# Kernel tuning notes

Hardware: AMD Instinct MI355X
Metric: run time of the kernel (lower is better)

Reference implementation:

```python
import jax, jax.numpy as jnp
import numpy as np

M = 4        # multi_anchor
B = 256      # graphs per batch
NPG = 64     # nodes per graph
N = B * NPG  # total nodes
DEG = 8
E = N * DEG
DF = 16      # raw node feature dim
D = 256      # emb_dim
L = 5        # num_layer
NA = 2       # num_anchor
TASKS = 10
T = 1.0


def _gnn_node(h, edge_src, edge_dst, gin_W1, gin_b1, gin_W2, gin_b2, eps):
    # GIN-style message passing: gather -> sum-scatter -> 2-layer MLP, per layer.
    for l in range(L):
        msg = h[:, edge_src]                                  # [M,E,D] gather
        agg = jnp.zeros_like(h).at[:, edge_dst].add(msg)      # [M,N,D] scatter-add
        z = (1.0 + eps[l]) * h + agg
        z = jax.nn.relu(z @ gin_W1[l] + gin_b1[l])
        h = jax.nn.relu(z @ gin_W2[l] + gin_b2[l])
    return h


def _mindist(h):
    # per-node min squared distance to other nodes in the same graph
    hg = h.reshape(M, B, NPG, D)
    sq = jnp.sum(hg * hg, axis=-1)                            # [M,B,n]
    d2 = sq[..., :, None] + sq[..., None, :] - 2.0 * jnp.einsum('mbid,mbjd->mbij', hg, hg)
    d2 = jnp.maximum(d2, 0.0) + jnp.eye(NPG, dtype=h.dtype) * 1e9
    return jnp.min(d2, axis=-1).reshape(M, N)


def reference(x, W_enc, b_enc, gin_W1, gin_b1, gin_W2, gin_b2, eps,
              anchor_emb, W_n2n, b_n2n, W_pred, b_pred, edge_src, edge_dst):
    # InputEncoder (float x -> MLP with tail activation)
    h0 = jax.nn.relu(x @ W_enc + b_enc)                       # [N,D]
    tx = jnp.broadcast_to(h0[None], (M, N, D))                # expand over multi_anchor
    anchor = jnp.zeros((M, N), dtype=jnp.int32)
    xcur = tx
    skey = jax.random.key(42)
    goff = jnp.arange(B) * NPG                                # graph offsets
    rows = jnp.arange(M)[:, None]
    for i in range(1, NA + 1):
        h = _gnn_node(xcur, edge_src, edge_dst, gin_W1, gin_b1, gin_W2, gin_b2, eps)
        mind = _mindist(h)                                    # [M,N]
        pred = -mind - 10.0 * (anchor > 0).astype(h.dtype)    # mask prior anchors
        logits = (pred * T).reshape(M, B, NPG)
        # categorical sample per (anchor-row, graph) via Gumbel-max == multinomial_sample_batch
        u = jax.random.uniform(jax.random.fold_in(skey, i), (M, B, NPG), minval=1e-9, maxval=1.0)
        idx = jnp.argmax(logits - jnp.log(-jnp.log(u)), axis=-1)  # [M,B]
        glob = idx + goff[None, :]
        anchor = anchor.at[rows, glob].set(i)
        xcur = tx * anchor_emb[anchor] + tx
    h = _gnn_node(xcur, edge_src, edge_dst, gin_W1, gin_b1, gin_W2, gin_b2, eps)
    hn = jax.nn.relu(h @ W_n2n + b_n2n)                       # node2node (tailact)
    hg = hn.reshape(M, B, NPG, D).mean(axis=2)                # mean graph pooling
    out = hg @ W_pred + b_pred                                # pred_lin
    return out.mean(axis=0)                                   # mean over multi_anchor -> [B,TASKS]


def setup_inputs():
    key = jax.random.key(0)
    ks = jax.random.split(key, 12)
    x = jax.random.normal(ks[0], (N, DF), dtype=jnp.float32)
    gid = jnp.repeat(jnp.arange(B), NPG * DEG)
    edge_src = gid * NPG + jax.random.randint(ks[1], (E,), 0, NPG)
    edge_dst = gid * NPG + jax.random.randint(ks[2], (E,), 0, NPG)
    s = lambda k, shp: (jax.random.normal(k, shp, dtype=jnp.float32) * 0.05)
    return {
        'x': x,
        'W_enc': s(ks[3], (DF, D)), 'b_enc': jnp.zeros((D,), jnp.float32),
        'gin_W1': s(ks[4], (L, D, D)), 'gin_b1': jnp.zeros((L, D), jnp.float32),
        'gin_W2': s(ks[5], (L, D, D)), 'gin_b2': jnp.zeros((L, D), jnp.float32),
        'eps': jnp.zeros((L,), jnp.float32),
        'anchor_emb': s(ks[6], (NA + 1, D)),
        'W_n2n': s(ks[7], (D, D)), 'b_n2n': jnp.zeros((D,), jnp.float32),
        'W_pred': s(ks[8], (D, TASKS)), 'b_pred': jnp.zeros((TASKS,), jnp.float32),
        'edge_src': edge_src, 'edge_dst': edge_dst,
    }
```

## Files before the change

kernel.cpp:

```cpp
#include <hip/hip_runtime.h>
#include <stdint.h>

typedef unsigned short u16;
typedef _Float16 f16;
typedef f16 f16x4 __attribute__((ext_vector_type(4)));
typedef f16 f16x8 __attribute__((ext_vector_type(8)));
typedef float f32x16 __attribute__((ext_vector_type(16)));

#define M_     4
#define B_     256
#define NPG_   64
#define N_     (B_*NPG_)
#define DEG_   8
#define E_     (N_*DEG_)
#define DF_    16
#define D_     256
#define L_     5
#define NA_    2
#define TASKS_ 10

#define HROW 520
#define TROW 136
#define MFMA16(a,b,c) __builtin_amdgcn_mfma_f32_32x32x16_f16(a,b,c,0,0,0)

__device__ __forceinline__ u16 h_bits(f16 h) { union { f16 h; u16 u; } c; c.h = h; return c.u; }
__device__ __forceinline__ f16 bits_h(u16 u) { union { u16 u; f16 h; } c; c.u = u; return c.h; }
__device__ __forceinline__ float h2f(u16 u) { return (float)bits_h(u); }
__device__ __forceinline__ void split_f16(float v, u16& hi, u16& lo) {
  f16 h = (f16)v;
  f16 l = (f16)(v - (float)h);
  hi = h_bits(h); lo = h_bits(l);
}

__device__ __forceinline__ int haddr8(int row, int chunk) {
  return row * HROW + ((chunk ^ (row & 7)) << 4);
}
__device__ __forceinline__ int taddr8(int d, int c) {
  return d * TROW + ((c ^ (d & 7)) << 4);
}

__device__ __forceinline__ uint32_t rotl32(uint32_t v, int r) { return (v << r) | (v >> (32 - r)); }
__device__ __forceinline__ void threefry2x32(uint32_t k0, uint32_t k1, uint32_t x0, uint32_t x1,
                                             uint32_t& o0, uint32_t& o1) {
  const uint32_t ks2 = k0 ^ k1 ^ 0x1BD11BDAu;
  x0 += k0; x1 += k1;
#define TFR(r) { x0 += x1; x1 = rotl32(x1, r); x1 ^= x0; }
  TFR(13) TFR(15) TFR(26) TFR(6)   x0 += k1;  x1 += ks2 + 1u;
  TFR(17) TFR(29) TFR(16) TFR(24)  x0 += ks2; x1 += k0 + 2u;
  TFR(13) TFR(15) TFR(26) TFR(6)   x0 += k0;  x1 += k1 + 3u;
  TFR(17) TFR(29) TFR(16) TFR(24)  x0 += k1;  x1 += ks2 + 4u;
  TFR(13) TFR(15) TFR(26) TFR(6)   x0 += ks2; x1 += k0 + 5u;
#undef TFR
  o0 = x0; o1 = x1;
}

template<int TERMS>
__device__ __forceinline__ void gemm_w_RT(u16* __restrict__ hfU, const u16* __restrict__ WTm,
                                          const float* __restrict__ bias, bool do_relu) {
  const int tid = threadIdx.x;
  const int lane = tid & 63, w = tid >> 6;
  const int l31 = lane & 31, lh = lane >> 5;
  const int col = w * 32 + l31;
  const float bv = bias ? bias[col] : 0.f;
  f32x16 acc0 = {}, acc1 = {};
  const u16* Bbase = WTm + col * 8;

  f16x8 ah0[3], ah1[3], al0[3], al1[3];
  f16x8 bh[4], bl[4];
  auto ldA = [&](int ks, int s) {
    const int chunk = ks * 2 + lh;
    const int a0 = haddr8(l31, chunk);
    const int a1 = haddr8(32 + l31, chunk);
    ah0[s] = *(const f16x8*)(hfU + a0);
    ah1[s] = *(const f16x8*)(hfU + a1);
    if (TERMS == 3) {
      al0[s] = *(const f16x8*)(hfU + a0 + 8);
      al1[s] = *(const f16x8*)(hfU + a1 + 8);
    }
  };
  auto ldB = [&](int ks, int s) {
    const int chunk = ks * 2 + lh;
    bh[s] = *(const f16x8*)(Bbase + chunk * 2048);
    if (TERMS == 3) bl[s] = *(const f16x8*)(Bbase + chunk * 2048 + 65536);
  };
  ldB(0, 0); ldB(1, 1); ldB(2, 2); ldA(0, 0); ldA(1, 1);
#pragma unroll
  for (int ks = 0; ks < 16; ++ks) {
    if (ks < 14) ldA(ks + 2, (ks + 2) % 3);
    if (ks < 13) ldB(ks + 3, (ks + 3) & 3);
    const int s = ks % 3, t = ks & 3;
    __builtin_amdgcn_s_setprio(1);
    if (TERMS == 3) {
      acc0 = MFMA16(ah0[s], bh[t], acc0);
      acc0 = MFMA16(ah0[s], bl[t], acc0);
      acc0 = MFMA16(al0[s], bh[t], acc0);
      acc1 = MFMA16(ah1[s], bh[t], acc1);
      acc1 = MFMA16(ah1[s], bl[t], acc1);
      acc1 = MFMA16(al1[s], bh[t], acc1);
    } else {
      acc0 = MFMA16(ah0[s], bh[t], acc0);
      acc1 = MFMA16(ah1[s], bh[t], acc1);
    }
    __builtin_amdgcn_s_setprio(0);
  }
  __syncthreads();
#pragma unroll
  for (int q = 0; q < 4; ++q) {
    f16x4 h4a, l4a, h4b, l4b;
#pragma unroll
    for (int e = 0; e < 4; ++e) {
      float v0 = acc0[q * 4 + e] + bv;
      float v1 = acc1[q * 4 + e] + bv;
      if (do_relu) { v0 = fmaxf(v0, 0.f); v1 = fmaxf(v1, 0.f); }
      if (TERMS == 3) {
        u16 hi, lo;
        split_f16(v0, hi, lo); h4a[e] = bits_h(hi); l4a[e] = bits_h(lo);
        split_f16(v1, hi, lo); h4b[e] = bits_h(hi); l4b[e] = bits_h(lo);
      } else {
        h4a[e] = (f16)v0; h4b[e] = (f16)v1;
      }
    }
    const int t0 = taddr8(col, q) + 4 * lh;
    const int t1 = taddr8(col, 4 + q) + 4 * lh;
    *(f16x4*)(hfU + t0) = h4a;
    *(f16x4*)(hfU + t1) = h4b;
    if (TERMS == 3) { *(f16x4*)(hfU + t0 + 8) = l4a; *(f16x4*)(hfU + t1 + 8) = l4b; }
  }
  __syncthreads();
}

template<int TERMS>
__device__ __forceinline__ void gemm_adj_TR(u16* __restrict__ hfU, const u16* __restrict__ AdjU,
                                            const float* __restrict__ bias, int slow,
                                            const float* __restrict__ diagC, float epsl) {
  const int tid = threadIdx.x;
  const int lane = tid & 63, w = tid >> 6;
  const int l31 = lane & 31, lh = lane >> 5;
  const int drow = w * 32 + l31;
  f32x16 acc0 = {}, acc1 = {};

  f16x8 uh[2], ul[2], B0[2], B1[2];
  auto ld = [&](int kk, int s) {
    const int chunk = kk * 2 + lh;
    const int ta = taddr8(drow, chunk);
    uh[s] = *(const f16x8*)(hfU + ta);
    if (TERMS == 3) ul[s] = *(const f16x8*)(hfU + ta + 8);
    B0[s] = *(const f16x8*)(AdjU + l31 * 72 + chunk * 8);
    B1[s] = *(const f16x8*)(AdjU + (32 + l31) * 72 + chunk * 8);
  };
  ld(0, 0);
#pragma unroll
  for (int kk = 0; kk < 4; ++kk) {
    if (kk < 3) ld(kk + 1, (kk + 1) & 1);
    const int s = kk & 1;
    __builtin_amdgcn_s_setprio(1);
    acc0 = MFMA16(uh[s], B0[s], acc0);
    acc1 = MFMA16(uh[s], B1[s], acc1);
    if (TERMS == 3) {
      acc0 = MFMA16(ul[s], B0[s], acc0);
      acc1 = MFMA16(ul[s], B1[s], acc1);
    }
    __builtin_amdgcn_s_setprio(0);
  }
  if (slow) {
    const int i0 = l31, i1 = 32 + l31;
    const float v0d = diagC[i0] + epsl, v1d = diagC[i1] + epsl;
    const float r0 = v0d - h2f(h_bits((f16)v0d));
    const float r1 = v1d - h2f(h_bits((f16)v1d));
#pragma unroll
    for (int r = 0; r < 16; ++r) {
      const int dp = w * 32 + (r & 3) + 8 * (r >> 2) + 4 * lh;
      const int a0 = taddr8(dp, i0 >> 3) + (i0 & 7);
      const int a1 = taddr8(dp, i1 >> 3) + (i1 & 7);
      float u0 = h2f(hfU[a0]);
      float u1 = h2f(hfU[a1]);
      if (TERMS == 3) { u0 += h2f(hfU[a0 + 8]); u1 += h2f(hfU[a1 + 8]); }
      acc0[r] += r0 * u0;
      acc1[r] += r1 * u1;
    }
  }
  __syncthreads();
#pragma unroll
  for (int q = 0; q < 4; ++q) {
    f16x4 h4a, l4a, h4b, l4b;
#pragma unroll
    for (int e = 0; e < 4; ++e) {
      const int r = q * 4 + e;
      const float bq = bias[w * 32 + 8 * q + 4 * lh + e];
      float v0 = fmaxf(acc0[r] + bq, 0.f);
      float v1 = fmaxf(acc1[r] + bq, 0.f);
      if (TERMS == 3) {
        u16 hi, lo;
        split_f16(v0, hi, lo); h4a[e] = bits_h(hi); l4a[e] = bits_h(lo);
        split_f16(v1, hi, lo); h4b[e] = bits_h(hi); l4b[e] = bits_h(lo);
      } else {
        h4a[e] = (f16)v0; h4b[e] = (f16)v1;
      }
    }
    const int c = w * 4 + q;
    const int a0 = haddr8(l31, c) + 4 * lh;
    const int a1 = haddr8(32 + l31, c) + 4 * lh;
    *(f16x4*)(hfU + a0) = h4a;
    *(f16x4*)(hfU + a1) = h4b;
    if (TERMS == 3) { *(f16x4*)(hfU + a0 + 8) = l4a; *(f16x4*)(hfU + a1 + 8) = l4b; }
  }
  __syncthreads();
}

template<int TERMS>
__device__ __forceinline__ void gemm_w_RR(u16* __restrict__ hfU, const u16* __restrict__ WTm,
                                          const float* __restrict__ bias, bool do_relu) {
  const int tid = threadIdx.x;
  const int lane = tid & 63, w = tid >> 6;
  const int l31 = lane & 31, lh = lane >> 5;
  f32x16 acc0 = {}, acc1 = {};
  const u16* Abase = WTm + (w * 32 + l31) * 8;

  f16x8 Wh[4], Wl[4];
  f16x8 Xh0[3], Xh1[3], Xl0[3], Xl1[3];
  auto ldW = [&](int ks, int s) {
    const int chunk = ks * 2 + lh;
    Wh[s] = *(const f16x8*)(Abase + chunk * 2048);
    if (TERMS == 3) Wl[s] = *(const f16x8*)(Abase + chunk * 2048 + 65536);
  };
  auto ldX = [&](int ks, int s) {
    const int chunk = ks * 2 + lh;
    const int b0 = haddr8(l31, chunk);
    const int b1_ = haddr8(32 + l31, chunk);
    Xh0[s] = *(const f16x8*)(hfU + b0);
    Xh1[s] = *(const f16x8*)(hfU + b1_);
    if (TERMS == 3) {
      Xl0[s] = *(const f16x8*)(hfU + b0 + 8);
      Xl1[s] = *(const f16x8*)(hfU + b1_ + 8);
    }
  };
  ldW(0, 0); ldW(1, 1); ldW(2, 2); ldX(0, 0); ldX(1, 1);
#pragma unroll
  for (int ks = 0; ks < 16; ++ks) {
    if (ks < 14) ldX(ks + 2, (ks + 2) % 3);
    if (ks < 13) ldW(ks + 3, (ks + 3) & 3);
    const int s = ks % 3, t = ks & 3;
    __builtin_amdgcn_s_setprio(1);
    if (TERMS == 3) {
      acc0 = MFMA16(Wh[t], Xh0[s], acc0);
      acc0 = MFMA16(Wl[t], Xh0[s], acc0);
      acc0 = MFMA16(Wh[t], Xl0[s], acc0);
      acc1 = MFMA16(Wh[t], Xh1[s], acc1);
      acc1 = MFMA16(Wl[t], Xh1[s], acc1);
      acc1 = MFMA16(Wh[t], Xl1[s], acc1);
    } else {
      acc0 = MFMA16(Wh[t], Xh0[s], acc0);
      acc1 = MFMA16(Wh[t], Xh1[s], acc1);
    }
    __builtin_amdgcn_s_setprio(0);
  }
  __syncthreads();
#pragma unroll
  for (int q = 0; q < 4; ++q) {
    f16x4 h4a, l4a, h4b, l4b;
#pragma unroll
    for (int e = 0; e < 4; ++e) {
      const int r = q * 4 + e;
      const float bq = bias[w * 32 + 8 * q + 4 * lh + e];
      float v0 = acc0[r] + bq;
      float v1 = acc1[r] + bq;
      if (do_relu) { v0 = fmaxf(v0, 0.f); v1 = fmaxf(v1, 0.f); }
      if (TERMS == 3) {
        u16 hi, lo;
        split_f16(v0, hi, lo); h4a[e] = bits_h(hi); l4a[e] = bits_h(lo);
        split_f16(v1, hi, lo); h4b[e] = bits_h(hi); l4b[e] = bits_h(lo);
      } else {
        h4a[e] = (f16)v0; h4b[e] = (f16)v1;
      }
    }
    const int c = w * 4 + q;
    const int a0 = haddr8(l31, c) + 4 * lh;
    const int a1 = haddr8(32 + l31, c) + 4 * lh;
    *(f16x4*)(hfU + a0) = h4a;
    *(f16x4*)(hfU + a1) = h4b;
    if (TERMS == 3) { *(f16x4*)(hfU + a0 + 8) = l4a; *(f16x4*)(hfU + a1 + 8) = l4b; }
  }
  __syncthreads();
}

__device__ __forceinline__ void mindist_mfma(u16* __restrict__ hfU, float* __restrict__ mindS) {
  const int tid = threadIdx.x;
  const int lane = tid & 63, w = tid >> 6;
  const int gb = w & 3, gi = gb >> 1, gj = gb & 1, ks = w >> 2;
  const int l31 = lane & 31, lh = lane >> 5;
  f32x16 acc = {};

  f16x8 Ah[2], Al[2], Bh[2], Bl[2];
  auto ld = [&](int t, int s) {
    const int chunk = 4 * t + 2 * ks + lh;
    const int ra = haddr8(gi * 32 + l31, chunk);
    const int rb_ = haddr8(gj * 32 + l31, chunk);
    Ah[s] = *(const f16x8*)(hfU + ra);
    Al[s] = *(const f16x8*)(hfU + ra + 8);
    Bh[s] = *(const f16x8*)(hfU + rb_);
    Bl[s] = *(const f16x8*)(hfU + rb_ + 8);
  };
  ld(0, 0);
#pragma unroll
  for (int t = 0; t < 8; ++t) {
    if (t < 7) ld(t + 1, (t + 1) & 1);
    const int s = t & 1;
    __builtin_amdgcn_s_setprio(1);
    acc = MFMA16(Ah[s], Bh[s], acc);
    acc = MFMA16(Ah[s], Bl[s], acc);
    acc = MFMA16(Al[s], Bh[s], acc);
    __builtin_amdgcn_s_setprio(0);
  }
  __syncthreads();
  float* hfF = (float*)hfU;
  if (ks == 1) {
#pragma unroll
    for (int r = 0; r < 16; ++r) {
      const int rr = (r & 3) + 8 * (r >> 2) + 4 * lh;
      hfF[gb * 1088 + rr * 34 + l31] = acc[r];
    }
  }
  __syncthreads();
  if (ks == 0) {
#pragma unroll
    for (int r = 0; r < 16; ++r) {
      const int rr = (r & 3) + 8 * (r >> 2) + 4 * lh;
      const float g = acc[r] + hfF[gb * 1088 + rr * 34 + l31];
      hfF[8192 + (gi * 32 + rr) * 66 + gj * 32 + l31] = g;
    }
  }
  __syncthreads();
  {
    const int i = tid >> 3, jt = tid & 7;
    const float gii = hfF[8192 + i * 66 + i];
    float dmin = 3.4e38f;
#pragma unroll
    for (int jj = 0; jj < 8; ++jj) {
      const int j = jt * 8 + jj;
      const float gjj = hfF[8192 + j * 66 + j];
      const float gij = hfF[8192 + i * 66 + j];
      float d2 = fmaxf(gii + gjj - 2.f * gij, 0.f);
      if (j == i) d2 += 1e9f;
      dmin = fminf(dmin, d2);
    }
    dmin = fminf(dmin, __shfl_xor(dmin, 1));
    dmin = fminf(dmin, __shfl_xor(dmin, 2));
    dmin = fminf(dmin, __shfl_xor(dmin, 4));
    if (jt == 0) mindS[i] = dmin;
  }
  __syncthreads();
}

__device__ __forceinline__ void stage_adj(u16* AdjU, const float* AdjF, int b, int tid) {
  const float* src = AdjF + b * 4096;
  for (int t = tid; t < 4096; t += 512)
    AdjU[(t >> 6) * 72 + (t & 63)] = h_bits((f16)src[t]);
}

template<bool WRITE_LO>
__device__ __forceinline__ void build_xcur(u16* hfU, const float* h0g, const float* aemb,
                                           const int* anchorS, int b, int tid) {
  const int i = tid >> 3, part = tid & 7;
  const float* t = h0g + (b * 64 + i) * 256;
  const float* e = aemb + anchorS[i] * D_;
#pragma unroll
  for (int c = 0; c < 4; ++c) {
    const int chunk = part * 4 + c;
    const float4 tv0 = *(const float4*)(t + chunk * 8);
    const float4 tv1 = *(const float4*)(t + chunk * 8 + 4);
    const float4 ev0 = *(const float4*)(e + chunk * 8);
    const float4 ev1 = *(const float4*)(e + chunk * 8 + 4);
    float vv[8];
    vv[0] = fmaf(tv0.x, ev0.x, tv0.x); vv[1] = fmaf(tv0.y, ev0.y, tv0.y);
    vv[2] = fmaf(tv0.z, ev0.z, tv0.z); vv[3] = fmaf(tv0.w, ev0.w, tv0.w);
    vv[4] = fmaf(tv1.x, ev1.x, tv1.x); vv[5] = fmaf(tv1.y, ev1.y, tv1.y);
    vv[6] = fmaf(tv1.z, ev1.z, tv1.z); vv[7] = fmaf(tv1.w, ev1.w, tv1.w);
    f16x8 hi8, lo8;
#pragma unroll
    for (int ee = 0; ee < 8; ++ee) { u16 h, l; split_f16(vv[ee], h, l); hi8[ee] = bits_h(h); lo8[ee] = bits_h(l); }
    const int a = haddr8(i, chunk);
    *(f16x8*)(hfU + a) = hi8;
    if (WRITE_LO) *(f16x8*)(hfU + a + 8) = lo8;
  }
}

__device__ __forceinline__ void sample_anchor(const float* mindS, float* scoreS, int* anchorS,
                                              int m, int b, int iter, int tid) {
  if (tid < 64) {
    const int j = tid;
    uint32_t k0, k1;
    threefry2x32(0u, 42u, 0u, (uint32_t)iter, k0, k1);
    const uint32_t p = (uint32_t)(m * (B_ * NPG_) + b * NPG_ + j);
    uint32_t o0, o1, bits;
    if (p < 32768u) { threefry2x32(k0, k1, p, p + 32768u, o0, o1); bits = o0; }
    else            { threefry2x32(k0, k1, p - 32768u, p, o0, o1); bits = o1; }
    const float f = __uint_as_float((bits >> 9) | 0x3f800000u) - 1.0f;
    const float uv = fmaxf(1e-9f, f + 1e-9f);
    const float pred = -mindS[j] - ((anchorS[j] > 0) ? 10.0f : 0.0f);
    scoreS[j] = pred - logf(-logf(uv));
  }
  __syncthreads();
  if (tid == 0) {
    int best = 0; float bv = scoreS[0];
    for (int j = 1; j < 64; ++j) { const float v = scoreS[j]; if (v > bv) { bv = v; best = j; } }
    anchorS[best] = iter;
  }
}

__global__ void build_adj_kernel(const int* __restrict__ esrc, const int* __restrict__ edst,
                                 float* __restrict__ AdjF) {
  const int e = blockIdx.x * 256 + threadIdx.x;
  if (e < E_) {
    const int s = esrc[e];
    const int d = edst[e];
    const int g = s >> 6;
    atomicAdd(AdjF + g * 4096 + (d & 63) * 64 + (s & 63), 1.0f);
  }
}

__global__ __launch_bounds__(256) void prep_wt(const float* __restrict__ gW1, const float* __restrict__ gW2,
                                               const float* __restrict__ Wn2n, u16* __restrict__ WTbuf) {
  const int mat = blockIdx.x;
  const float* Wsrc = (mat < 5) ? (gW1 + mat * 65536)
                    : (mat < 10) ? (gW2 + (mat - 5) * 65536) : Wn2n;
  u16* dst = WTbuf + (size_t)mat * 131072;
  const int base = blockIdx.y * 2048;
  for (int idx = base + threadIdx.x; idx < base + 2048; idx += 256) {
    const int k = idx >> 8, d = idx & 255;
    const float a = Wsrc[idx];
    u16 hi, lo; split_f16(a, hi, lo);
    const int off = (k >> 3) * 2048 + d * 8 + (k & 7);
    dst[off] = hi;
    dst[65536 + off] = lo;
  }
}

__global__ __launch_bounds__(512)
void gnn1_kernel(const float* __restrict__ x, const float* __restrict__ Wenc,
                 const float* __restrict__ benc, float* __restrict__ h0g,
                 const float* __restrict__ AdjF, const u16* __restrict__ WTbuf,
                 const float* __restrict__ gb1, const float* __restrict__ gb2,
                 const float* __restrict__ eps, float* __restrict__ mindG) {
  __shared__ __align__(16) u16 hfU[256 * TROW];
  __shared__ __align__(16) u16 AdjU[64 * 72];
  __shared__ float mindS[64];
  __shared__ float diagC[64];
  __shared__ int flagS;
  const int tid = threadIdx.x;
  const int b = blockIdx.x;

  {
    float* scr = (float*)hfU;
    for (int t = tid; t < 4096; t += 512) {
      const int k = t >> 8, d = t & 255;
      scr[k * 264 + d + (d >> 5)] = Wenc[t];
    }
    if (tid < 256) scr[4300 + tid] = benc[tid];
    for (int t = tid; t < 1024; t += 512) scr[4600 + t] = x[b * 1024 + t];
    __syncthreads();

    const int i = tid >> 3, part = tid & 7;
    float xv[16];
#pragma unroll
    for (int k = 0; k < 16; ++k) xv[k] = scr[4600 + i * 16 + k];
    float hv[32];
#pragma unroll
    for (int dd = 0; dd < 32; ++dd) {
      const int d = part * 32 + dd;
      float acc = scr[4300 + d];
#pragma unroll
      for (int k = 0; k < 16; ++k) acc = fmaf(xv[k], scr[k * 264 + d + (d >> 5)], acc);
      hv[dd] = fmaxf(acc, 0.f);
    }
    float* dst = h0g + (b * 64 + i) * 256 + part * 32;
#pragma unroll
    for (int dd = 0; dd < 32; dd += 4) {
      float4 v; v.x = hv[dd]; v.y = hv[dd + 1]; v.z = hv[dd + 2]; v.w = hv[dd + 3];
      *(float4*)(dst + dd) = v;
    }
    __syncthreads();
#pragma unroll
    for (int c = 0; c < 4; ++c) {
      f16x8 hi8, lo8;
#pragma unroll
      for (int e = 0; e < 8; ++e) { u16 h, l; split_f16(hv[c * 8 + e], h, l); hi8[e] = bits_h(h); lo8[e] = bits_h(l); }
      const int a = haddr8(i, part * 4 + c);
      *(f16x8*)(hfU + a) = hi8;
      *(f16x8*)(hfU + a + 8) = lo8;
    }
  }
  stage_adj(AdjU, AdjF, b, tid);
  if (tid == 0) flagS = 0;
  if (tid < 64) {
    const float dc = AdjF[b * 4096 + tid * 65];
    diagC[tid] = dc;
    int f = 0;
    for (int l = 0; l < L_; ++l) {
      const float v = dc + 1.0f + eps[l];
      if (h2f(h_bits((f16)v)) != v) f = 1;
    }
    if (f) atomicOr(&flagS, 1);
  }
  __syncthreads();
  const int slow = flagS;

  for (int l = 0; l < L_; ++l) {
    const float epsl = 1.0f + eps[l];
    if (tid < 64) AdjU[tid * 72 + tid] = h_bits((f16)(diagC[tid] + epsl));
    gemm_w_RT<3>(hfU, WTbuf + (size_t)l * 131072, nullptr, false);
    gemm_adj_TR<3>(hfU, AdjU, gb1 + l * D_, slow, diagC, epsl);
    gemm_w_RR<3>(hfU, WTbuf + (size_t)(5 + l) * 131072, gb2 + l * D_, true);
  }
  mindist_mfma(hfU, mindS);
  if (tid < 64) mindG[b * 64 + tid] = mindS[tid];
}

__global__ __launch_bounds__(512, 4)
void mega_kernel(const float* __restrict__ h0g, const float* __restrict__ AdjF,
                 const u16* __restrict__ WTbuf,
                 const float* __restrict__ gb1, const float* __restrict__ gb2,
                 const float* __restrict__ eps, const float* __restrict__ aemb,
                 const float* __restrict__ bn2n,
                 const float* __restrict__ Wpred, const float* __restrict__ bpred,
                 const float* __restrict__ mindG, float* __restrict__ outp) {
  __shared__ __align__(16) u16 hfU[256 * TROW];
  __shared__ __align__(16) u16 AdjU[64 * 72];
  __shared__ float mindS[64];
  __shared__ float scoreS[64];
  __shared__ float hgS[256];
  __shared__ int   anchorS[64];
  __shared__ float diagC[64];
  __shared__ int   flagS;

  const int tid = threadIdx.x;
  const int b = blockIdx.x;
  const int m = blockIdx.y;

  stage_adj(AdjU, AdjF, b, tid);
  if (tid == 0) flagS = 0;
  if (tid < 64) {
    anchorS[tid] = 0;
    mindS[tid] = mindG[b * 64 + tid];
    const float dc = AdjF[b * 4096 + tid * 65];
    diagC[tid] = dc;
    int f = 0;
    for (int l = 0; l < L_; ++l) {
      const float v = dc + 1.0f + eps[l];
      if (h2f(h_bits((f16)v)) != v) f = 1;
    }
    if (f) atomicOr(&flagS, 1);
  }
  __syncthreads();

  sample_anchor(mindS, scoreS, anchorS, m, b, 1, tid);
  __syncthreads();
  build_xcur<true>(hfU, h0g, aemb, anchorS, b, tid);
  __syncthreads();

  const int slow = flagS;

  for (int l = 0; l < L_; ++l) {
    const float epsl = 1.0f + eps[l];
    if (tid < 64) AdjU[tid * 72 + tid] = h_bits((f16)(diagC[tid] + epsl));
    gemm_w_RT<3>(hfU, WTbuf + (size_t)l * 131072, nullptr, false);
    gemm_adj_TR<3>(hfU, AdjU, gb1 + l * D_, slow, diagC, epsl);
    gemm_w_RR<3>(hfU, WTbuf + (size_t)(5 + l) * 131072, gb2 + l * D_, true);
  }
  mindist_mfma(hfU, mindS);
  sample_anchor(mindS, scoreS, anchorS, m, b, 2, tid);
  __syncthreads();
  build_xcur<false>(hfU, h0g, aemb, anchorS, b, tid);
  __syncthreads();

  for (int l = 0; l < L_; ++l) {
    const float epsl = 1.0f + eps[l];
    if (tid < 64) AdjU[tid * 72 + tid] = h_bits((f16)(diagC[tid] + epsl));
    gemm_w_RT<1>(hfU, WTbuf + (size_t)l * 131072, nullptr, false);
    gemm_adj_TR<1>(hfU, AdjU, gb1 + l * D_, slow, diagC, epsl);
    gemm_w_RR<1>(hfU, WTbuf + (size_t)(5 + l) * 131072, gb2 + l * D_, true);
  }

  gemm_w_RT<1>(hfU, WTbuf + (size_t)10 * 131072, bn2n, true);
  if (tid < 256) {
    float s = 0.f;
#pragma unroll
    for (int c = 0; c < 8; ++c) {
      const f16x8 v = *(const f16x8*)(hfU + taddr8(tid, c));
      s += (float)v[0] + (float)v[1] + (float)v[2] + (float)v[3]
         + (float)v[4] + (float)v[5] + (float)v[6] + (float)v[7];
    }
    hgS[tid] = s * (1.0f / 64.0f);
  }
  __syncthreads();
  if (tid < 160) {
    const int t = tid >> 4, part = tid & 15;
    float s = 0.f;
    for (int d = part * 16; d < part * 16 + 16; ++d) s = fmaf(hgS[d], Wpred[d * TASKS_ + t], s);
    s += __shfl_xor(s, 1); s += __shfl_xor(s, 2); s += __shfl_xor(s, 4); s += __shfl_xor(s, 8);
    if (part == 0) {
      float val = s * 0.25f;
      if (m == 0) val += bpred[t];
      atomicAdd(outp + b * TASKS_ + t, val);
    }
  }
}

extern "C" void kernel_launch(void* const* d_in, const int* in_sizes, int n_in,
                              void* d_out, int out_size, void* d_ws, size_t ws_size,
                              hipStream_t stream) {
  const float* x     = (const float*)d_in[0];
  const float* Wenc  = (const float*)d_in[1];
  const float* benc  = (const float*)d_in[2];
  const float* gW1   = (const float*)d_in[3];
  const float* gb1   = (const float*)d_in[4];
  const float* gW2   = (const float*)d_in[5];
  const float* gb2   = (const float*)d_in[6];
  const float* eps   = (const float*)d_in[7];
  const float* aemb  = (const float*)d_in[8];
  const float* Wn2n  = (const float*)d_in[9];
  const float* bn2n  = (const float*)d_in[10];
  const float* Wpred = (const float*)d_in[11];
  const float* bpred = (const float*)d_in[12];
  const int* esrc    = (const int*)d_in[13];
  const int* edst    = (const int*)d_in[14];
  float* outp = (float*)d_out;

  float* h0g  = (float*)d_ws;
  float* AdjF = h0g + (size_t)N_ * D_;
  u16* WTbuf  = (u16*)(AdjF + B_ * 4096);
  float* mindG = (float*)(WTbuf + (size_t)11 * 131072);

  hipMemsetAsync(AdjF, 0, (size_t)B_ * 4096 * sizeof(float), stream);
  hipMemsetAsync(outp, 0, (size_t)out_size * sizeof(float), stream);
  build_adj_kernel<<<dim3((E_ + 255) / 256), dim3(256), 0, stream>>>(esrc, edst, AdjF);
  prep_wt<<<dim3(11, 32), dim3(256), 0, stream>>>(gW1, gW2, Wn2n, WTbuf);
  gnn1_kernel<<<dim3(B_), dim3(512), 0, stream>>>(x, Wenc, benc, h0g, AdjF, WTbuf,
                                                  gb1, gb2, eps, mindG);
  mega_kernel<<<dim3(B_, M_), dim3(512), 0, stream>>>(h0g, AdjF, WTbuf, gb1, gb2,
                                                      eps, aemb, bn2n, Wpred, bpred, mindG, outp);
}
```

Before: 714.7 us.

## Ping-pong LDS buffers to drop mid-GEMM barriers and interleave MFMA chains

Replaces the single in-place shared activation buffer with two ping-pong buffers, so each GEMM stage reads one buffer and writes the other. This removes the barrier that separated the last read from the epilogue write in every GEMM and in mindist. It also interleaves the acc0/acc1 MFMA chains to reduce dependency stalls, and sets launch bounds to one block. The cost is double the LDS per block (about 140KB), which likely limits occupancy to one 512-thread block per CU.

```diff
diff --git a/kernel.cpp b/kernel.cpp
--- a/kernel.cpp
+++ b/kernel.cpp
@@ -21,6 +21,7 @@
 
 #define HROW 520
 #define TROW 136
+#define BUFW (256 * TROW)
 #define MFMA16(a,b,c) __builtin_amdgcn_mfma_f32_32x32x16_f16(a,b,c,0,0,0)
 
 __device__ __forceinline__ u16 h_bits(f16 h) { union { f16 h; u16 u; } c; c.h = h; return c.u; }
@@ -55,7 +56,8 @@
 }
 
 template<int TERMS>
-__device__ __forceinline__ void gemm_w_RT(u16* __restrict__ hfU, const u16* __restrict__ WTm,
+__device__ __forceinline__ void gemm_w_RT(const u16* __restrict__ rbuf, u16* __restrict__ wbuf,
+                                          const u16* __restrict__ WTm,
                                           const float* __restrict__ bias, bool do_relu) {
   const int tid = threadIdx.x;
   const int lane = tid & 63, w = tid >> 6;
@@ -71,11 +73,11 @@
     const int chunk = ks * 2 + lh;
     const int a0 = haddr8(l31, chunk);
     const int a1 = haddr8(32 + l31, chunk);
-    ah0[s] = *(const f16x8*)(hfU + a0);
-    ah1[s] = *(const f16x8*)(hfU + a1);
+    ah0[s] = *(const f16x8*)(rbuf + a0);
+    ah1[s] = *(const f16x8*)(rbuf + a1);
     if (TERMS == 3) {
-      al0[s] = *(const f16x8*)(hfU + a0 + 8);
-      al1[s] = *(const f16x8*)(hfU + a1 + 8);
+      al0[s] = *(const f16x8*)(rbuf + a0 + 8);
+      al1[s] = *(const f16x8*)(rbuf + a1 + 8);
     }
   };
   auto ldB = [&](int ks, int s) {
@@ -92,10 +94,10 @@
     __builtin_amdgcn_s_setprio(1);
     if (TERMS == 3) {
       acc0 = MFMA16(ah0[s], bh[t], acc0);
+      acc1 = MFMA16(ah1[s], bh[t], acc1);
       acc0 = MFMA16(ah0[s], bl[t], acc0);
+      acc1 = MFMA16(ah1[s], bl[t], acc1);
       acc0 = MFMA16(al0[s], bh[t], acc0);
-      acc1 = MFMA16(ah1[s], bh[t], acc1);
-      acc1 = MFMA16(ah1[s], bl[t], acc1);
       acc1 = MFMA16(al1[s], bh[t], acc1);
     } else {
       acc0 = MFMA16(ah0[s], bh[t], acc0);
@@ -103,7 +105,6 @@
     }
     __builtin_amdgcn_s_setprio(0);
   }
-  __syncthreads();
 #pragma unroll
   for (int q = 0; q < 4; ++q) {
     f16x4 h4a, l4a, h4b, l4b;
@@ -122,15 +123,16 @@
     }
     const int t0 = taddr8(col, q) + 4 * lh;
     const int t1 = taddr8(col, 4 + q) + 4 * lh;
-    *(f16x4*)(hfU + t0) = h4a;
-    *(f16x4*)(hfU + t1) = h4b;
-    if (TERMS == 3) { *(f16x4*)(hfU + t0 + 8) = l4a; *(f16x4*)(hfU + t1 + 8) = l4b; }
+    *(f16x4*)(wbuf + t0) = h4a;
+    *(f16x4*)(wbuf + t1) = h4b;
+    if (TERMS == 3) { *(f16x4*)(wbuf + t0 + 8) = l4a; *(f16x4*)(wbuf + t1 + 8) = l4b; }
   }
   __syncthreads();
 }
 
 template<int TERMS>
-__device__ __forceinline__ void gemm_adj_TR(u16* __restrict__ hfU, const u16* __restrict__ AdjU,
+__device__ __forceinline__ void gemm_adj_TR(const u16* __restrict__ rbuf, u16* __restrict__ wbuf,
+                                            const u16* __restrict__ AdjU,
                                             const float* __restrict__ bias, int slow,
                                             const float* __restrict__ diagC, float epsl) {
   const int tid = threadIdx.x;
@@ -143,8 +145,8 @@
   auto ld = [&](int kk, int s) {
     const int chunk = kk * 2 + lh;
     const int ta = taddr8(drow, chunk);
-    uh[s] = *(const f16x8*)(hfU + ta);
-    if (TERMS == 3) ul[s] = *(const f16x8*)(hfU + ta + 8);
+    uh[s] = *(const f16x8*)(rbuf + ta);
+    if (TERMS == 3) ul[s] = *(const f16x8*)(rbuf + ta + 8);
     B0[s] = *(const f16x8*)(AdjU + l31 * 72 + chunk * 8);
     B1[s] = *(const f16x8*)(AdjU + (32 + l31) * 72 + chunk * 8);
   };
@@ -172,14 +174,13 @@
       const int dp = w * 32 + (r & 3) + 8 * (r >> 2) + 4 * lh;
       const int a0 = taddr8(dp, i0 >> 3) + (i0 & 7);
       const int a1 = taddr8(dp, i1 >> 3) + (i1 & 7);
-      float u0 = h2f(hfU[a0]);
-      float u1 = h2f(hfU[a1]);
-      if (TERMS == 3) { u0 += h2f(hfU[a0 + 8]); u1 += h2f(hfU[a1 + 8]); }
+      float u0 = h2f(rbuf[a0]);
+      float u1 = h2f(rbuf[a1]);
+      if (TERMS == 3) { u0 += h2f(rbuf[a0 + 8]); u1 += h2f(rbuf[a1 + 8]); }
       acc0[r] += r0 * u0;
       acc1[r] += r1 * u1;
     }
   }
-  __syncthreads();
 #pragma unroll
   for (int q = 0; q < 4; ++q) {
     f16x4 h4a, l4a, h4b, l4b;
@@ -200,15 +201,16 @@
     const int c = w * 4 + q;
     const int a0 = haddr8(l31, c) + 4 * lh;
     const int a1 = haddr8(32 + l31, c) + 4 * lh;
-    *(f16x4*)(hfU + a0) = h4a;
-    *(f16x4*)(hfU + a1) = h4b;
-    if (TERMS == 3) { *(f16x4*)(hfU + a0 + 8) = l4a; *(f16x4*)(hfU + a1 + 8) = l4b; }
+    *(f16x4*)(wbuf + a0) = h4a;
+    *(f16x4*)(wbuf + a1) = h4b;
+    if (TERMS == 3) { *(f16x4*)(wbuf + a0 + 8) = l4a; *(f16x4*)(wbuf + a1 + 8) = l4b; }
   }
   __syncthreads();
 }
 
 template<int TERMS>
-__device__ __forceinline__ void gemm_w_RR(u16* __restrict__ hfU, const u16* __restrict__ WTm,
+__device__ __forceinline__ void gemm_w_RR(const u16* __restrict__ rbuf, u16* __restrict__ wbuf,
+                                          const u16* __restrict__ WTm,
                                           const float* __restrict__ bias, bool do_relu) {
   const int tid = threadIdx.x;
   const int lane = tid & 63, w = tid >> 6;
@@ -227,11 +229,11 @@
     const int chunk = ks * 2 + lh;
     const int b0 = haddr8(l31, chunk);
     const int b1_ = haddr8(32 + l31, chunk);
-    Xh0[s] = *(const f16x8*)(hfU + b0);
-    Xh1[s] = *(const f16x8*)(hfU + b1_);
+    Xh0[s] = *(const f16x8*)(rbuf + b0);
+    Xh1[s] = *(const f16x8*)(rbuf + b1_);
     if (TERMS == 3) {
-      Xl0[s] = *(const f16x8*)(hfU + b0 + 8);
-      Xl1[s] = *(const f16x8*)(hfU + b1_ + 8);
+      Xl0[s] = *(const f16x8*)(rbuf + b0 + 8);
+      Xl1[s] = *(const f16x8*)(rbuf + b1_ + 8);
     }
   };
   ldW(0, 0); ldW(1, 1); ldW(2, 2); ldX(0, 0); ldX(1, 1);
@@ -243,10 +245,10 @@
     __builtin_amdgcn_s_setprio(1);
     if (TERMS == 3) {
       acc0 = MFMA16(Wh[t], Xh0[s], acc0);
+      acc1 = MFMA16(Wh[t], Xh1[s], acc1);
       acc0 = MFMA16(Wl[t], Xh0[s], acc0);
+      acc1 = MFMA16(Wl[t], Xh1[s], acc1);
       acc0 = MFMA16(Wh[t], Xl0[s], acc0);
-      acc1 = MFMA16(Wh[t], Xh1[s], acc1);
-      acc1 = MFMA16(Wl[t], Xh1[s], acc1);
       acc1 = MFMA16(Wh[t], Xl1[s], acc1);
     } else {
       acc0 = MFMA16(Wh[t], Xh0[s], acc0);
@@ -254,7 +256,6 @@
     }
     __builtin_amdgcn_s_setprio(0);
   }
-  __syncthreads();
 #pragma unroll
   for (int q = 0; q < 4; ++q) {
     f16x4 h4a, l4a, h4b, l4b;
@@ -276,14 +277,15 @@
     const int c = w * 4 + q;
     const int a0 = haddr8(l31, c) + 4 * lh;
     const int a1 = haddr8(32 + l31, c) + 4 * lh;
-    *(f16x4*)(hfU + a0) = h4a;
-    *(f16x4*)(hfU + a1) = h4b;
-    if (TERMS == 3) { *(f16x4*)(hfU + a0 + 8) = l4a; *(f16x4*)(hfU + a1 + 8) = l4b; }
-  }
-  __syncthreads();
-}
-
-__device__ __forceinline__ void mindist_mfma(u16* __restrict__ hfU, float* __restrict__ mindS) {
+    *(f16x4*)(wbuf + a0) = h4a;
+    *(f16x4*)(wbuf + a1) = h4b;
+    if (TERMS == 3) { *(f16x4*)(wbuf + a0 + 8) = l4a; *(f16x4*)(wbuf + a1 + 8) = l4b; }
+  }
+  __syncthreads();
+}
+
+__device__ __forceinline__ void mindist_mfma(const u16* __restrict__ rbuf, u16* __restrict__ scr,
+                                             float* __restrict__ mindS) {
   const int tid = threadIdx.x;
   const int lane = tid & 63, w = tid >> 6;
   const int gb = w & 3, gi = gb >> 1, gj = gb & 1, ks = w >> 2;
@@ -295,10 +297,10 @@
     const int chunk = 4 * t + 2 * ks + lh;
     const int ra = haddr8(gi * 32 + l31, chunk);
     const int rb_ = haddr8(gj * 32 + l31, chunk);
-    Ah[s] = *(const f16x8*)(hfU + ra);
-    Al[s] = *(const f16x8*)(hfU + ra + 8);
-    Bh[s] = *(const f16x8*)(hfU + rb_);
-    Bl[s] = *(const f16x8*)(hfU + rb_ + 8);
+    Ah[s] = *(const f16x8*)(rbuf + ra);
+    Al[s] = *(const f16x8*)(rbuf + ra + 8);
+    Bh[s] = *(const f16x8*)(rbuf + rb_);
+    Bl[s] = *(const f16x8*)(rbuf + rb_ + 8);
   };
   ld(0, 0);
 #pragma unroll
@@ -311,8 +313,7 @@
     acc = MFMA16(Al[s], Bh[s], acc);
     __builtin_amdgcn_s_setprio(0);
   }
-  __syncthreads();
-  float* hfF = (float*)hfU;
+  float* hfF = (float*)scr;
   if (ks == 1) {
 #pragma unroll
     for (int r = 0; r < 16; ++r) {
@@ -358,7 +359,7 @@
 }
 
 template<bool WRITE_LO>
-__device__ __forceinline__ void build_xcur(u16* hfU, const float* h0g, const float* aemb,
+__device__ __forceinline__ void build_xcur(u16* dst, const float* h0g, const float* aemb,
                                            const int* anchorS, int b, int tid) {
   const int i = tid >> 3, part = tid & 7;
   const float* t = h0g + (b * 64 + i) * 256;
@@ -379,8 +380,8 @@
 #pragma unroll
     for (int ee = 0; ee < 8; ++ee) { u16 h, l; split_f16(vv[ee], h, l); hi8[ee] = bits_h(h); lo8[ee] = bits_h(l); }
     const int a = haddr8(i, chunk);
-    *(f16x8*)(hfU + a) = hi8;
-    if (WRITE_LO) *(f16x8*)(hfU + a + 8) = lo8;
+    *(f16x8*)(dst + a) = hi8;
+    if (WRITE_LO) *(f16x8*)(dst + a + 8) = lo8;
   }
 }
 
@@ -435,13 +436,14 @@
   }
 }
 
-__global__ __launch_bounds__(512)
+__global__ __launch_bounds__(512, 1)
 void gnn1_kernel(const float* __restrict__ x, const float* __restrict__ Wenc,
                  const float* __restrict__ benc, float* __restrict__ h0g,
                  const float* __restrict__ AdjF, const u16* __restrict__ WTbuf,
                  const float* __restrict__ gb1, const float* __restrict__ gb2,
                  const float* __restrict__ eps, float* __restrict__ mindG) {
-  __shared__ __align__(16) u16 hfU[256 * TROW];
+  __shared__ __align__(16) u16 bufA[BUFW];
+  __shared__ __align__(16) u16 bufB[BUFW];
   __shared__ __align__(16) u16 AdjU[64 * 72];
   __shared__ float mindS[64];
   __shared__ float diagC[64];
@@ -450,7 +452,7 @@
   const int b = blockIdx.x;
 
   {
-    float* scr = (float*)hfU;
+    float* scr = (float*)bufB;
     for (int t = tid; t < 4096; t += 512) {
       const int k = t >> 8, d = t & 255;
       scr[k * 264 + d + (d >> 5)] = Wenc[t];
@@ -478,15 +480,14 @@
       float4 v; v.x = hv[dd]; v.y = hv[dd + 1]; v.z = hv[dd + 2]; v.w = hv[dd + 3];
       *(float4*)(dst + dd) = v;
     }
-    __syncthreads();
 #pragma unroll
     for (int c = 0; c < 4; ++c) {
       f16x8 hi8, lo8;
 #pragma unroll
       for (int e = 0; e < 8; ++e) { u16 h, l; split_f16(hv[c * 8 + e], h, l); hi8[e] = bits_h(h); lo8[e] = bits_h(l); }
       const int a = haddr8(i, part * 4 + c);
-      *(f16x8*)(hfU + a) = hi8;
-      *(f16x8*)(hfU + a + 8) = lo8;
+      *(f16x8*)(bufA + a) = hi8;
+      *(f16x8*)(bufA + a + 8) = lo8;
     }
   }
   stage_adj(AdjU, AdjF, b, tid);
@@ -504,18 +505,21 @@
   __syncthreads();
   const int slow = flagS;
 
+  u16* cur = bufA;
+  u16* alt = bufB;
   for (int l = 0; l < L_; ++l) {
     const float epsl = 1.0f + eps[l];
     if (tid < 64) AdjU[tid * 72 + tid] = h_bits((f16)(diagC[tid] + epsl));
-    gemm_w_RT<3>(hfU, WTbuf + (size_t)l * 131072, nullptr, false);
-    gemm_adj_TR<3>(hfU, AdjU, gb1 + l * D_, slow, diagC, epsl);
-    gemm_w_RR<3>(hfU, WTbuf + (size_t)(5 + l) * 131072, gb2 + l * D_, true);
-  }
-  mindist_mfma(hfU, mindS);
+    gemm_w_RT<3>(cur, alt, WTbuf + (size_t)l * 131072, nullptr, false);
+    gemm_adj_TR<3>(alt, cur, AdjU, gb1 + l * D_, slow, diagC, epsl);
+    gemm_w_RR<3>(cur, alt, WTbuf + (size_t)(5 + l) * 131072, gb2 + l * D_, true);
+    u16* t = cur; cur = alt; alt = t;
+  }
+  mindist_mfma(cur, alt, mindS);
   if (tid < 64) mindG[b * 64 + tid] = mindS[tid];
 }
 
-__global__ __launch_bounds__(512, 4)
+__global__ __launch_bounds__(512, 1)
 void mega_kernel(const float* __restrict__ h0g, const float* __restrict__ AdjF,
                  const u16* __restrict__ WTbuf,
                  const float* __restrict__ gb1, const float* __restrict__ gb2,
@@ -523,7 +527,8 @@
                  const float* __restrict__ bn2n,
                  const float* __restrict__ Wpred, const float* __restrict__ bpred,
                  const float* __restrict__ mindG, float* __restrict__ outp) {
-  __shared__ __align__(16) u16 hfU[256 * TROW];
+  __shared__ __align__(16) u16 bufA[BUFW];
+  __shared__ __align__(16) u16 bufB[BUFW];
   __shared__ __align__(16) u16 AdjU[64 * 72];
   __shared__ float mindS[64];
   __shared__ float scoreS[64];
@@ -554,7 +559,9 @@
 
   sample_anchor(mindS, scoreS, anchorS, m, b, 1, tid);
   __syncthreads();
-  build_xcur<true>(hfU, h0g, aemb, anchorS, b, tid);
+  u16* cur = bufA;
+  u16* alt = bufB;
+  build_xcur<true>(cur, h0g, aemb, anchorS, b, tid);
   __syncthreads();
 
   const int slow = flagS;
@@ -562,30 +569,32 @@
   for (int l = 0; l < L_; ++l) {
     const float epsl = 1.0f + eps[l];
     if (tid < 64) AdjU[tid * 72 + tid] = h_bits((f16)(diagC[tid] + epsl));
-    gemm_w_RT<3>(hfU, WTbuf + (size_t)l * 131072, nullptr, false);
-    gemm_adj_TR<3>(hfU, AdjU, gb1 + l * D_, slow, diagC, epsl);
-    gemm_w_RR<3>(hfU, WTbuf + (size_t)(5 + l) * 131072, gb2 + l * D_, true);
-  }
-  mindist_mfma(hfU, mindS);
+    gemm_w_RT<3>(cur, alt, WTbuf + (size_t)l * 131072, nullptr, false);
+    gemm_adj_TR<3>(alt, cur, AdjU, gb1 + l * D_, slow, diagC, epsl);
+    gemm_w_RR<3>(cur, alt, WTbuf + (size_t)(5 + l) * 131072, gb2 + l * D_, true);
+    u16* t = cur; cur = alt; alt = t;
+  }
+  mindist_mfma(cur, alt, mindS);
   sample_anchor(mindS, scoreS, anchorS, m, b, 2, tid);
   __syncthreads();
-  build_xcur<false>(hfU, h0g, aemb, anchorS, b, tid);
+  build_xcur<false>(cur, h0g, aemb, anchorS, b, tid);
   __syncthreads();
 
   for (int l = 0; l < L_; ++l) {
     const float epsl = 1.0f + eps[l];
     if (tid < 64) AdjU[tid * 72 + tid] = h_bits((f16)(diagC[tid] + epsl));
-    gemm_w_RT<1>(hfU, WTbuf + (size_t)l * 131072, nullptr, false);
-    gemm_adj_TR<1>(hfU, AdjU, gb1 + l * D_, slow, diagC, epsl);
-    gemm_w_RR<1>(hfU, WTbuf + (size_t)(5 + l) * 131072, gb2 + l * D_, true);
-  }
-
-  gemm_w_RT<1>(hfU, WTbuf + (size_t)10 * 131072, bn2n, true);
+    gemm_w_RT<1>(cur, alt, WTbuf + (size_t)l * 131072, nullptr, false);
+    gemm_adj_TR<1>(alt, cur, AdjU, gb1 + l * D_, slow, diagC, epsl);
+    gemm_w_RR<1>(cur, alt, WTbuf + (size_t)(5 + l) * 131072, gb2 + l * D_, true);
+    u16* t = cur; cur = alt; alt = t;
+  }
+
+  gemm_w_RT<1>(cur, alt, WTbuf + (size_t)10 * 131072, bn2n, true);
   if (tid < 256) {
     float s = 0.f;
 #pragma unroll
     for (int c = 0; c < 8; ++c) {
-      const f16x8 v = *(const f16x8*)(hfU + taddr8(tid, c));
+      const f16x8 v = *(const f16x8*)(alt + taddr8(tid, c));
       s += (float)v[0] + (float)v[1] + (float)v[2] + (float)v[3]
          + (float)v[4] + (float)v[5] + (float)v[6] + (float)v[7];
     }
```

Result: faster. 588.5 us (-17.6%).
